# Kernel optimization log

Measured on AMD Instinct MI355X. Metric: run time of the kernel, lower is better.

Reference implementation:

```python
import jax, jax.numpy as jnp
import numpy as np

B, S, D, H = 4, 2048, 1024, 16
HD = D // H
THETA = 10000.0


def rope(x, pos, theta=THETA):
    # x: [..., seq, d], pos: broadcastable to [..., seq]
    d = x.shape[-1]
    half = d // 2
    inv_freq = 1.0 / (theta ** (jnp.arange(half, dtype=jnp.float32) * 2.0 / d))  # [half]
    ang = pos[..., None].astype(jnp.float32) * inv_freq  # [..., seq, half]
    cos, sin = jnp.cos(ang), jnp.sin(ang)
    x1, x2 = x[..., 0::2], x[..., 1::2]
    r1 = x1 * cos - x2 * sin
    r2 = x1 * sin + x2 * cos
    return jnp.stack([r1, r2], axis=-1).reshape(x.shape).astype(x.dtype)


def setup_inputs() -> dict:
    key = jax.random.key(0)
    ks = jax.random.split(key, 5)
    x = jax.random.normal(ks[0], (B, S, D), dtype=jnp.float32)
    token_positions = jnp.tile(jnp.arange(S, dtype=jnp.int64 if jax.config.jax_enable_x64 else jnp.int32), (B, 1))
    scale = 0.02
    Wq = jax.random.normal(ks[1], (D, D), dtype=jnp.float32) * scale
    Wk = jax.random.normal(ks[2], (D, D), dtype=jnp.float32) * scale
    Wv = jax.random.normal(ks[3], (D, D), dtype=jnp.float32) * scale
    Wo = jax.random.normal(ks[4], (D, D), dtype=jnp.float32) * scale
    return {"x": x, "token_positions": token_positions, "Wq": Wq, "Wk": Wk, "Wv": Wv, "Wo": Wo}


def reference(x, token_positions, Wq, Wk, Wv, Wo):
    b, s, d = x.shape
    # QKV projections (torch Linear: x @ W.T), split heads -> [b, h, s, hd]
    def proj(W):
        y = jnp.einsum('bsd,ed->bse', x, W)
        return y.reshape(b, s, H, HD).transpose(0, 2, 1, 3)
    Q, K, V = proj(Wq), proj(Wk), proj(Wv)
    # token_positions [..., seq] -> [..., 1, seq] to broadcast over heads
    pos = token_positions[:, None, :]  # [b, 1, s]
    Q = rope(Q, pos)
    K = rope(K, pos)
    # causal mask and scaled dot-product attention
    idx = jnp.arange(s)
    causal = idx[:, None] >= idx[None, :]  # [s, s], query >= key
    scores = jnp.einsum('bhqd,bhkd->bhqk', Q, K) / jnp.sqrt(jnp.float32(HD))
    scores = jnp.where(causal, scores, -jnp.inf)
    weights = jax.nn.softmax(scores, axis=-1)
    o = jnp.einsum('bhqk,bhkd->bhqd', weights, V)
    o = o.transpose(0, 2, 1, 3).reshape(b, s, d)  # merge heads
    return jnp.einsum('bsd,ed->bse', o, Wo)
```

## Files before the change

kernel.cpp:

```cpp
#include <hip/hip_runtime.h>

#define S_LEN 2048
#define NH 16
#define HDIM 64
#define DMODEL 1024

typedef __attribute__((ext_vector_type(8))) short bf16x8;
typedef __attribute__((ext_vector_type(4))) float f32x4;

__device__ __forceinline__ short f2bf(float f) {
    union { float f; unsigned u; } x; x.f = f;
    unsigned r = x.u + 0x7fffu + ((x.u >> 16) & 1u);
    return (short)(r >> 16);
}

#define GLDS(g, l) __builtin_amdgcn_global_load_lds( \
    (__attribute__((address_space(1))) void*)(g),    \
    (__attribute__((address_space(3))) void*)(l), 16, 0, 0)

#define QSCALE 0.18033688011112042f
#define FREQ_L 0.41524101186109327f

__global__ __launch_bounds__(256) void prep(const float* __restrict__ x,
                                            const float* __restrict__ wq,
                                            const float* __restrict__ wk,
                                            const float* __restrict__ wv,
                                            const float* __restrict__ wo,
                                            const int* __restrict__ tp,
                                            short* __restrict__ xb,
                                            short* __restrict__ wqb,
                                            short* __restrict__ wkb,
                                            short* __restrict__ wvb,
                                            short* __restrict__ wob,
                                            float2* __restrict__ tab) {
    int bid = blockIdx.x;
    if (bid < 8192) {
        int i = bid * 256 + threadIdx.x;
        float4 v = ((const float4*)x)[i];
        short4 o;
        o.x = f2bf(v.x); o.y = f2bf(v.y); o.z = f2bf(v.z); o.w = f2bf(v.w);
        ((short4*)xb)[i] = o;
    } else if (bid < 12288) {
        int sel = (bid - 8192) >> 10;
        const float* in = sel == 0 ? wq : sel == 1 ? wk : sel == 2 ? wv : wo;
        short* out = sel == 0 ? wqb : sel == 1 ? wkb : sel == 2 ? wvb : wob;
        int i = ((bid - 8192) & 1023) * 256 + threadIdx.x;
        float4 v = ((const float4*)in)[i];
        short4 o;
        o.x = f2bf(v.x); o.y = f2bf(v.y); o.z = f2bf(v.z); o.w = f2bf(v.w);
        ((short4*)out)[i] = o;
    } else {
        int idx = (bid - 12288) * 256 + threadIdx.x;
        int b = idx >> 16, s = (idx >> 5) & 2047, i = idx & 31;
        float p = (float)tp[(b << 11) + s];
        float freq = exp2f(-(float)i * FREQ_L);
        float sn, cs;
        sincosf(p * freq, &sn, &cs);
        tab[idx] = make_float2(cs, sn);
    }
}

__global__ __launch_bounds__(512) void gemm_qkv(const short* __restrict__ A,
                                                const short* __restrict__ Bq,
                                                const short* __restrict__ Bk,
                                                const short* __restrict__ Bv,
                                                const float2* __restrict__ tab,
                                                short* __restrict__ Qo,
                                                short* __restrict__ Ko,
                                                short* __restrict__ Vo) {
    constexpr int K = 1024;
    __shared__ __align__(16) short smem[3 * 12288];

    const int bm = blockIdx.x;
    const int sel = blockIdx.y >> 3;
    const int bn = blockIdx.y & 7;
    const short* Bm = sel == 0 ? Bq : sel == 1 ? Bk : Bv;
    short* Cb = sel == 0 ? Qo : sel == 1 ? Ko : Vo;

    const int tid = threadIdx.x;
    const int lane = tid & 63;
    const int w = tid >> 6;
    const int wm = w >> 1;
    const int wn = w & 1;
    const int quad = lane >> 4, l16 = lane & 15;

    int aoff[2], boffv;
#pragma unroll
    for (int i = 0; i < 2; i++) {
        int Lc = i * 512 + tid;
        int row = Lc >> 2;
        int gc = (Lc & 3) ^ ((row >> 1) & 3);
        aoff[i] = (bm * 256 + row) * K + gc * 8;
    }
    {
        int row = tid >> 2;
        int gc = (tid & 3) ^ ((row >> 1) & 3);
        boffv = (bn * 128 + row) * K + gc * 8;
    }

    auto stage = [&](int h, int slot) {
        char* sbase = (char*)smem + slot * 24576;
        const int kh = h * 32;
#pragma unroll
        for (int i = 0; i < 2; i++)
            GLDS(A + aoff[i] + kh, sbase + i * 8192 + w * 1024);
        GLDS(Bm + boffv + kh, sbase + 16384 + w * 1024);
    };

    f32x4 acc[4][4] = {};
    const int rsw = (quad ^ ((l16 >> 1) & 3)) * 8;

    auto compute = [&](int slot) {
        const short* sA = smem + slot * 12288;
        const short* sB = sA + 8192;
        bf16x8 af[4], bfm[4];
#pragma unroll
        for (int mi = 0; mi < 4; mi++)
            af[mi] = *(const bf16x8*)&sA[(wm * 64 + mi * 16 + l16) * 32 + rsw];
#pragma unroll
        for (int ni = 0; ni < 4; ni++)
            bfm[ni] = *(const bf16x8*)&sB[(wn * 64 + ni * 16 + l16) * 32 + rsw];
        __builtin_amdgcn_s_setprio(1);
#pragma unroll
        for (int mi = 0; mi < 4; mi++)
#pragma unroll
            for (int ni = 0; ni < 4; ni++)
                acc[mi][ni] = __builtin_amdgcn_mfma_f32_16x16x32_bf16(af[mi], bfm[ni],
                                                                      acc[mi][ni], 0, 0, 0);
        __builtin_amdgcn_s_setprio(0);
    };

    stage(0, 0); stage(1, 1);

    auto step = [&](int h, int sc, int ss) {
        asm volatile("s_waitcnt vmcnt(3)" ::: "memory");
        __builtin_amdgcn_s_barrier();
        __builtin_amdgcn_sched_barrier(0);
        stage(h + 2, ss);
        compute(sc);
    };

    for (int h = 0; h < 30; h += 3) {
        step(h + 0, 0, 2);
        step(h + 1, 1, 0);
        step(h + 2, 2, 1);
    }
    asm volatile("s_waitcnt vmcnt(3)" ::: "memory");
    __builtin_amdgcn_s_barrier();
    __builtin_amdgcn_sched_barrier(0);
    compute(0);
    asm volatile("s_waitcnt vmcnt(0)" ::: "memory");
    __builtin_amdgcn_s_barrier();
    __builtin_amdgcn_sched_barrier(0);
    compute(1);

    const int gm0 = bm * 256 + wm * 64;
    const int gn0 = bn * 128 + wn * 64;

    if (sel == 2) {
        short* T = smem;
        __syncthreads();
#pragma unroll
        for (int mi = 0; mi < 4; mi++) {
            int lmb = wm * 64 + mi * 16 + quad * 4;
#pragma unroll
            for (int ni = 0; ni < 4; ni++) {
                int ln = wn * 64 + ni * 16 + l16;
                short4 pk;
                pk.x = f2bf(acc[mi][ni][0]);
                pk.y = f2bf(acc[mi][ni][1]);
                pk.z = f2bf(acc[mi][ni][2]);
                pk.w = f2bf(acc[mi][ni][3]);
                *(short4*)&T[ln * 256 + (lmb ^ ((ln & 31) << 3))] = pk;
            }
        }
        __syncthreads();
        const int row = tid >> 2, qt = tid & 3;
        const int grow = bn * 128 + row;
        const int gb = bm >> 3;
        const int gs0 = (bm & 7) * 256;
        short* dst = Cb + (((size_t)(gb * NH + (grow >> 6)) * HDIM + (grow & 63)) * S_LEN
                           + gs0 + qt * 64);
#pragma unroll
        for (int j = 0; j < 8; j++) {
            bf16x8 v = *(const bf16x8*)&T[row * 256 +
                        ((qt * 64 + j * 8) ^ ((row & 31) << 3))];
            *(bf16x8*)(dst + j * 8) = v;
        }
    } else {
        const float qs = (sel == 0) ? QSCALE : 1.0f;
#pragma unroll
        for (int mi = 0; mi < 4; mi++)
#pragma unroll
            for (int r = 0; r < 4; r++) {
                int gm = gm0 + mi * 16 + quad * 4 + r;
                const float2* trow = tab + (gm << 5);
                int b = gm >> 11, s = gm & 2047;
#pragma unroll
                for (int ni = 0; ni < 4; ni++) {
                    float2 cs = trow[ni * 8 + (l16 >> 1)];
                    float v = acc[mi][ni][r];
                    float prt = __shfl_xor(v, 1, 64);
                    float val = (l16 & 1) ? (prt * cs.y + v * cs.x)
                                          : (v * cs.x - prt * cs.y);
                    int gn = gn0 + ni * 16 + l16;
                    int h = gn >> 6, hd = gn & 63;
                    Cb[((b * NH + h) * S_LEN + s) * HDIM + hd] = f2bf(val * qs);
                }
            }
    }
}

__global__ __launch_bounds__(512) void gemm_o(const short* __restrict__ A,
                                              const short* __restrict__ Bw,
                                              float* __restrict__ Cf) {
    constexpr int K = 1024, N = 1024;
    __shared__ __align__(16) short smem[3 * 8192];

    const int bm = blockIdx.x;
    const int bn = blockIdx.y;

    const int tid = threadIdx.x;
    const int lane = tid & 63;
    const int w = tid >> 6;
    const int wm = w >> 2;
    const int wn = w & 3;
    const int quad = lane >> 4, l16 = lane & 15;

    int aoffv, boffv;
    {
        int row = tid >> 2;
        int gc = (tid & 3) ^ ((row >> 1) & 3);
        aoffv = (bm * 128 + row) * K + gc * 8;
        boffv = (bn * 128 + row) * K + gc * 8;
    }

    auto stage = [&](int h, int slot) {
        char* sbase = (char*)smem + slot * 16384;
        const int kh = h * 32;
        GLDS(A + aoffv + kh, sbase + w * 1024);
        GLDS(Bw + boffv + kh, sbase + 8192 + w * 1024);
    };

    f32x4 acc[4][2] = {};
    const int rsw = (quad ^ ((l16 >> 1) & 3)) * 8;

    auto compute = [&](int slot) {
        const short* sA = smem + slot * 8192;
        const short* sB = sA + 4096;
        bf16x8 af[4], bfm[2];
#pragma unroll
        for (int mi = 0; mi < 4; mi++)
            af[mi] = *(const bf16x8*)&sA[(wm * 64 + mi * 16 + l16) * 32 + rsw];
#pragma unroll
        for (int ni = 0; ni < 2; ni++)
            bfm[ni] = *(const bf16x8*)&sB[(wn * 32 + ni * 16 + l16) * 32 + rsw];
        __builtin_amdgcn_s_setprio(1);
#pragma unroll
        for (int mi = 0; mi < 4; mi++)
#pragma unroll
            for (int ni = 0; ni < 2; ni++)
                acc[mi][ni] = __builtin_amdgcn_mfma_f32_16x16x32_bf16(af[mi], bfm[ni],
                                                                      acc[mi][ni], 0, 0, 0);
        __builtin_amdgcn_s_setprio(0);
    };

    stage(0, 0); stage(1, 1);

    auto step = [&](int h, int sc, int ss) {
        asm volatile("s_waitcnt vmcnt(2)" ::: "memory");
        __builtin_amdgcn_s_barrier();
        __builtin_amdgcn_sched_barrier(0);
        stage(h + 2, ss);
        compute(sc);
    };

    for (int h = 0; h < 30; h += 3) {
        step(h + 0, 0, 2);
        step(h + 1, 1, 0);
        step(h + 2, 2, 1);
    }
    asm volatile("s_waitcnt vmcnt(2)" ::: "memory");
    __builtin_amdgcn_s_barrier();
    __builtin_amdgcn_sched_barrier(0);
    compute(0);
    asm volatile("s_waitcnt vmcnt(0)" ::: "memory");
    __builtin_amdgcn_s_barrier();
    __builtin_amdgcn_sched_barrier(0);
    compute(1);

    const int gm0 = bm * 128 + wm * 64;
    const int gn0 = bn * 128 + wn * 32;
#pragma unroll
    for (int mi = 0; mi < 4; mi++)
#pragma unroll
        for (int ni = 0; ni < 2; ni++)
#pragma unroll
            for (int r = 0; r < 4; r++) {
                int gm = gm0 + mi * 16 + quad * 4 + r;
                int gn = gn0 + ni * 16 + l16;
                Cf[gm * N + gn] = acc[mi][ni][r];
            }
}

__global__ __launch_bounds__(256, 2) void attn(const short* __restrict__ Q,
                                               const short* __restrict__ Km,
                                               const short* __restrict__ Vt,
                                               short* __restrict__ O) {
    __shared__ __align__(16) short kbuf[3][64 * 64];
    __shared__ __align__(16) short vbuf[3][64 * 64];
    __shared__ __align__(16) short pbuf[4][32 * 64];

    const int lane = threadIdx.x & 63;
    const int w = threadIdx.x >> 6;
    const int quad = lane >> 4, l16 = lane & 15;
    const int l7 = l16 & 7;
    const int bh = blockIdx.x;

    const short* Qg = Q  + bh * S_LEN * 64;
    const short* Kg = Km + bh * S_LEN * 64;
    const short* Vg = Vt + bh * 64 * S_LEN;
    short* myp = &pbuf[w][0];

    const int b = bh >> 4, h = bh & 15;

    bf16x8 ones;
#pragma unroll
    for (int j = 0; j < 8; j++) ones[j] = (short)0x3f80;

    auto stage = [&](int kt, int slot) {
        const short* kt_base = Kg + kt * 64 * 64;
        const short* vt_base = Vg + kt * 64;
#pragma unroll
        for (int i = 0; i < 2; ++i) {
            int ch = w * 128 + i * 64 + lane;
            int row = ch >> 3;
            int c = (ch & 7) ^ (row & 7);
            GLDS(kt_base + row * 64 + c * 8, (char*)&kbuf[slot][(w * 128 + i * 64) * 8]);
        }
#pragma unroll
        for (int i = 0; i < 2; ++i) {
            int ch = w * 128 + i * 64 + lane;
            int row = ch >> 3;
            int c = (ch & 7) ^ (row & 7);
            GLDS(vt_base + row * S_LEN + c * 8, (char*)&vbuf[slot][(w * 128 + i * 64) * 8]);
        }
    };

    const int QtA = blockIdx.y;
    const int QtB = 15 - blockIdx.y;

    bf16x8 apA[2][2], apB[2][2];
    int s0 = 0;
    stage(0, 0);

    for (int phase = 0; phase < 2; ++phase) {
        const int Qt = phase ? QtB : QtA;
        const int nkt = 2 * Qt + 2;

        bf16x8 aq[2][2];
#pragma unroll
        for (int mi = 0; mi < 2; mi++) {
            int qrow = Qt * 128 + w * 32 + mi * 16 + l16;
#pragma unroll
            for (int kc = 0; kc < 2; kc++)
                aq[mi][kc] = *(const bf16x8*)&Qg[qrow * 64 + kc * 32 + quad * 8];
        }

        f32x4 oacc[2][4] = {};
        f32x4 lacc[2] = {};

        auto iter = [&](int kt, int scur, int snext, int sprev,
                        bf16x8 (&apc)[2][2], bf16x8 (&app)[2][2], bool hasPrev) {
            __syncthreads();
            int stk = kt + 1;
            if (stk < nkt)       stage(stk, snext);
            else if (phase == 0) stage(0,   snext);
            const short* kb = &kbuf[scur][0];
            const short* vb = &vbuf[sprev][0];

            f32x4 sc[2][4] = {};
            __builtin_amdgcn_s_setprio(1);
#pragma unroll
            for (int nt = 0; nt < 4; nt++) {
                int raddr = (nt * 16 + l16) * 64;
#pragma unroll
                for (int kc = 0; kc < 2; kc++) {
                    bf16x8 kf = *(const bf16x8*)&kb[raddr + (((quad + kc * 4) ^ l7) * 8)];
                    sc[0][nt] = __builtin_amdgcn_mfma_f32_16x16x32_bf16(aq[0][kc], kf, sc[0][nt], 0, 0, 0);
                    sc[1][nt] = __builtin_amdgcn_mfma_f32_16x16x32_bf16(aq[1][kc], kf, sc[1][nt], 0, 0, 0);
                }
            }
            if (hasPrev) {
#pragma unroll
                for (int nt = 0; nt < 4; nt++) {
                    int raddr = (nt * 16 + l16) * 64;
#pragma unroll
                    for (int kc = 0; kc < 2; kc++) {
                        bf16x8 vf = *(const bf16x8*)&vb[raddr + (((quad + kc * 4) ^ l7) * 8)];
                        oacc[0][nt] = __builtin_amdgcn_mfma_f32_16x16x32_bf16(app[0][kc], vf, oacc[0][nt], 0, 0, 0);
                        oacc[1][nt] = __builtin_amdgcn_mfma_f32_16x16x32_bf16(app[1][kc], vf, oacc[1][nt], 0, 0, 0);
                    }
                }
#pragma unroll
                for (int mi = 0; mi < 2; mi++) {
                    lacc[mi] = __builtin_amdgcn_mfma_f32_16x16x32_bf16(app[mi][0], ones, lacc[mi], 0, 0, 0);
                    lacc[mi] = __builtin_amdgcn_mfma_f32_16x16x32_bf16(app[mi][1], ones, lacc[mi], 0, 0, 0);
                }
            }
            __builtin_amdgcn_s_setprio(0);

            if (kt >= nkt - 2) {
#pragma unroll
                for (int mi = 0; mi < 2; mi++)
#pragma unroll
                    for (int nt = 0; nt < 4; nt++)
#pragma unroll
                        for (int r = 0; r < 4; r++) {
                            int col = kt * 64 + nt * 16 + l16;
                            int row = Qt * 128 + w * 32 + mi * 16 + quad * 4 + r;
                            if (col > row) sc[mi][nt][r] = -__builtin_inff();
                        }
            }
#pragma unroll
            for (int mi = 0; mi < 2; mi++)
#pragma unroll
                for (int nt = 0; nt < 4; nt++)
#pragma unroll
                    for (int r = 0; r < 4; r++) {
                        float pv = __builtin_amdgcn_exp2f(sc[mi][nt][r]);
                        int q = mi * 16 + quad * 4 + r;
                        union { float f; unsigned short us[2]; } uu;
                        uu.f = pv;
                        myp[q * 64 + (((nt * 2 + (l16 >> 3)) ^ (q & 7)) * 8) + l7] =
                            (short)uu.us[1];
                    }
#pragma unroll
            for (int mi = 0; mi < 2; mi++)
#pragma unroll
                for (int kc = 0; kc < 2; kc++)
                    apc[mi][kc] = *(const bf16x8*)&myp[(mi * 16 + l16) * 64 +
                                                       (((quad + kc * 4) ^ l7) * 8)];
        };

        for (int kt = 0; kt < nkt; kt += 2) {
            int s1 = s0 + 1; if (s1 == 3) s1 = 0;
            int s2 = s1 + 1; if (s2 == 3) s2 = 0;
            iter(kt,     s0, s1, s2, apA, apB, kt > 0);
            iter(kt + 1, s1, s2, s0, apB, apA, true);
            s0 = s2;
        }
        {
            int slast = s0 - 1; if (slast < 0) slast = 2;
            const short* vb = &vbuf[slast][0];
            __builtin_amdgcn_s_setprio(1);
#pragma unroll
            for (int nt = 0; nt < 4; nt++) {
                int raddr = (nt * 16 + l16) * 64;
#pragma unroll
                for (int kc = 0; kc < 2; kc++) {
                    bf16x8 vf = *(const bf16x8*)&vb[raddr + (((quad + kc * 4) ^ l7) * 8)];
                    oacc[0][nt] = __builtin_amdgcn_mfma_f32_16x16x32_bf16(apB[0][kc], vf, oacc[0][nt], 0, 0, 0);
                    oacc[1][nt] = __builtin_amdgcn_mfma_f32_16x16x32_bf16(apB[1][kc], vf, oacc[1][nt], 0, 0, 0);
                }
            }
#pragma unroll
            for (int mi = 0; mi < 2; mi++) {
                lacc[mi] = __builtin_amdgcn_mfma_f32_16x16x32_bf16(apB[mi][0], ones, lacc[mi], 0, 0, 0);
                lacc[mi] = __builtin_amdgcn_mfma_f32_16x16x32_bf16(apB[mi][1], ones, lacc[mi], 0, 0, 0);
            }
            __builtin_amdgcn_s_setprio(0);
        }
#pragma unroll
        for (int mi = 0; mi < 2; mi++)
#pragma unroll
            for (int r = 0; r < 4; r++) {
                float inv = 1.0f / lacc[mi][r];
                int srow = Qt * 128 + w * 32 + mi * 16 + quad * 4 + r;
#pragma unroll
                for (int nt = 0; nt < 4; nt++) {
                    int hd = nt * 16 + l16;
                    O[(b * S_LEN + srow) * DMODEL + h * HDIM + hd] = f2bf(oacc[mi][nt][r] * inv);
                }
            }
    }
}

extern "C" void kernel_launch(void* const* d_in, const int* in_sizes, int n_in,
                              void* d_out, int out_size, void* d_ws, size_t ws_size,
                              hipStream_t stream) {
    const float* x  = (const float*)d_in[0];
    const int*   tp = (const int*)d_in[1];
    const float* Wq = (const float*)d_in[2];
    const float* Wk = (const float*)d_in[3];
    const float* Wv = (const float*)d_in[4];
    const float* Wo = (const float*)d_in[5];
    float* out = (float*)d_out;

    char* ws = (char*)d_ws;
    const size_t MB = 1024 * 1024;
    short* xb  = (short*)(ws);
    short* wqb = (short*)(ws + 16 * MB);
    short* wkb = (short*)(ws + 18 * MB);
    short* wvb = (short*)(ws + 20 * MB);
    short* wob = (short*)(ws + 22 * MB);
    short* Qb  = (short*)(ws + 24 * MB);
    short* Kb  = (short*)(ws + 40 * MB);
    short* Vtb = (short*)(ws + 56 * MB);
    float2* tab = (float2*)d_out;

    prep<<<13312, 256, 0, stream>>>(x, Wq, Wk, Wv, Wo, tp,
                                    xb, wqb, wkb, wvb, wob, tab);

    gemm_qkv<<<dim3(32, 24), 512, 0, stream>>>(xb, wqb, wkb, wvb, tab, Qb, Kb, Vtb);

    attn<<<dim3(64, 8), 256, 0, stream>>>(Qb, Kb, Vtb, xb);

    gemm_o<<<dim3(64, 8), 512, 0, stream>>>(xb, wob, out);
}
```

Before: 235.1 us.

## Split attention into one query tile per block with double-buffered K/V

The attention kernel previously had each block handle two paired query tiles (Qt and 15-Qt) for load balance, with a three-slot K/V ring and a software-pipelined P·V stage lagging one iteration. It now launches 16 blocks per head, one query tile each, uses two K/V buffers, and runs QK, softmax and PV in the same iteration. Launch bounds rise to 3 blocks per CU to use the freed shared memory. The goal is more occupancy and parallelism, but it gives up the paired-tile load balancing and the overlap of PV with the next QK, and puts the K/V load for the next tile directly behind the barrier.

```diff
diff --git a/kernel.cpp b/kernel.cpp
--- a/kernel.cpp
+++ b/kernel.cpp
@@ -303,12 +303,12 @@
             }
 }
 
-__global__ __launch_bounds__(256, 2) void attn(const short* __restrict__ Q,
+__global__ __launch_bounds__(256, 3) void attn(const short* __restrict__ Q,
                                                const short* __restrict__ Km,
                                                const short* __restrict__ Vt,
                                                short* __restrict__ O) {
-    __shared__ __align__(16) short kbuf[3][64 * 64];
-    __shared__ __align__(16) short vbuf[3][64 * 64];
+    __shared__ __align__(16) short kbuf[2][64 * 64];
+    __shared__ __align__(16) short vbuf[2][64 * 64];
     __shared__ __align__(16) short pbuf[4][32 * 64];
 
     const int lane = threadIdx.x & 63;
@@ -328,7 +328,7 @@
 #pragma unroll
     for (int j = 0; j < 8; j++) ones[j] = (short)0x3f80;
 
-    auto stage = [&](int kt, int slot) {
+    auto stage = [&](int kt, int par) {
         const short* kt_base = Kg + kt * 64 * 64;
         const short* vt_base = Vg + kt * 64;
 #pragma unroll
@@ -336,154 +336,115 @@
             int ch = w * 128 + i * 64 + lane;
             int row = ch >> 3;
             int c = (ch & 7) ^ (row & 7);
-            GLDS(kt_base + row * 64 + c * 8, (char*)&kbuf[slot][(w * 128 + i * 64) * 8]);
+            GLDS(kt_base + row * 64 + c * 8, (char*)&kbuf[par][(w * 128 + i * 64) * 8]);
         }
 #pragma unroll
         for (int i = 0; i < 2; ++i) {
             int ch = w * 128 + i * 64 + lane;
             int row = ch >> 3;
             int c = (ch & 7) ^ (row & 7);
-            GLDS(vt_base + row * S_LEN + c * 8, (char*)&vbuf[slot][(w * 128 + i * 64) * 8]);
-        }
-    };
-
-    const int QtA = blockIdx.y;
-    const int QtB = 15 - blockIdx.y;
-
-    bf16x8 apA[2][2], apB[2][2];
-    int s0 = 0;
+            GLDS(vt_base + row * S_LEN + c * 8, (char*)&vbuf[par][(w * 128 + i * 64) * 8]);
+        }
+    };
+
+    const int Qt = 15 - blockIdx.y;
+    const int nkt = 2 * Qt + 2;
+
     stage(0, 0);
 
-    for (int phase = 0; phase < 2; ++phase) {
-        const int Qt = phase ? QtB : QtA;
-        const int nkt = 2 * Qt + 2;
-
-        bf16x8 aq[2][2];
+    bf16x8 aq[2][2];
+#pragma unroll
+    for (int mi = 0; mi < 2; mi++) {
+        int qrow = Qt * 128 + w * 32 + mi * 16 + l16;
+#pragma unroll
+        for (int kc = 0; kc < 2; kc++)
+            aq[mi][kc] = *(const bf16x8*)&Qg[qrow * 64 + kc * 32 + quad * 8];
+    }
+
+    f32x4 oacc[2][4] = {};
+    f32x4 lacc[2] = {};
+
+    for (int kt = 0; kt < nkt; ++kt) {
+        __syncthreads();
+        if (kt + 1 < nkt) stage(kt + 1, (kt + 1) & 1);
+        const short* kb_cur = &kbuf[kt & 1][0];
+        const short* vb_cur = &vbuf[kt & 1][0];
+
+        f32x4 sc[2][4] = {};
+        __builtin_amdgcn_s_setprio(1);
+#pragma unroll
+        for (int nt = 0; nt < 4; nt++) {
+            int raddr = (nt * 16 + l16) * 64;
+#pragma unroll
+            for (int kc = 0; kc < 2; kc++) {
+                bf16x8 kf = *(const bf16x8*)&kb_cur[raddr + (((quad + kc * 4) ^ l7) * 8)];
+                sc[0][nt] = __builtin_amdgcn_mfma_f32_16x16x32_bf16(aq[0][kc], kf, sc[0][nt], 0, 0, 0);
+                sc[1][nt] = __builtin_amdgcn_mfma_f32_16x16x32_bf16(aq[1][kc], kf, sc[1][nt], 0, 0, 0);
+            }
+        }
+        __builtin_amdgcn_s_setprio(0);
+        if (kt >= nkt - 2) {
+#pragma unroll
+            for (int mi = 0; mi < 2; mi++)
+#pragma unroll
+                for (int nt = 0; nt < 4; nt++)
+#pragma unroll
+                    for (int r = 0; r < 4; r++) {
+                        int col = kt * 64 + nt * 16 + l16;
+                        int row = Qt * 128 + w * 32 + mi * 16 + quad * 4 + r;
+                        if (col > row) sc[mi][nt][r] = -__builtin_inff();
+                    }
+        }
+#pragma unroll
+        for (int mi = 0; mi < 2; mi++)
+#pragma unroll
+            for (int nt = 0; nt < 4; nt++)
+#pragma unroll
+                for (int r = 0; r < 4; r++) {
+                    float pv = __builtin_amdgcn_exp2f(sc[mi][nt][r]);
+                    int q = mi * 16 + quad * 4 + r;
+                    union { float f; unsigned short us[2]; } uu;
+                    uu.f = pv;
+                    myp[q * 64 + (((nt * 2 + (l16 >> 3)) ^ (q & 7)) * 8) + l7] =
+                        (short)uu.us[1];
+                }
+        bf16x8 ap[2][2];
+#pragma unroll
+        for (int mi = 0; mi < 2; mi++)
+#pragma unroll
+            for (int kc = 0; kc < 2; kc++)
+                ap[mi][kc] = *(const bf16x8*)&myp[(mi * 16 + l16) * 64 +
+                                                  (((quad + kc * 4) ^ l7) * 8)];
+        __builtin_amdgcn_s_setprio(1);
+#pragma unroll
+        for (int nt = 0; nt < 4; nt++) {
+            int raddr = (nt * 16 + l16) * 64;
+#pragma unroll
+            for (int kc = 0; kc < 2; kc++) {
+                bf16x8 vf = *(const bf16x8*)&vb_cur[raddr + (((quad + kc * 4) ^ l7) * 8)];
+                oacc[0][nt] = __builtin_amdgcn_mfma_f32_16x16x32_bf16(ap[0][kc], vf, oacc[0][nt], 0, 0, 0);
+                oacc[1][nt] = __builtin_amdgcn_mfma_f32_16x16x32_bf16(ap[1][kc], vf, oacc[1][nt], 0, 0, 0);
+            }
+        }
 #pragma unroll
         for (int mi = 0; mi < 2; mi++) {
-            int qrow = Qt * 128 + w * 32 + mi * 16 + l16;
-#pragma unroll
-            for (int kc = 0; kc < 2; kc++)
-                aq[mi][kc] = *(const bf16x8*)&Qg[qrow * 64 + kc * 32 + quad * 8];
-        }
-
-        f32x4 oacc[2][4] = {};
-        f32x4 lacc[2] = {};
-
-        auto iter = [&](int kt, int scur, int snext, int sprev,
-                        bf16x8 (&apc)[2][2], bf16x8 (&app)[2][2], bool hasPrev) {
-            __syncthreads();
-            int stk = kt + 1;
-            if (stk < nkt)       stage(stk, snext);
-            else if (phase == 0) stage(0,   snext);
-            const short* kb = &kbuf[scur][0];
-            const short* vb = &vbuf[sprev][0];
-
-            f32x4 sc[2][4] = {};
-            __builtin_amdgcn_s_setprio(1);
+            lacc[mi] = __builtin_amdgcn_mfma_f32_16x16x32_bf16(ap[mi][0], ones, lacc[mi], 0, 0, 0);
+            lacc[mi] = __builtin_amdgcn_mfma_f32_16x16x32_bf16(ap[mi][1], ones, lacc[mi], 0, 0, 0);
+        }
+        __builtin_amdgcn_s_setprio(0);
+    }
+#pragma unroll
+    for (int mi = 0; mi < 2; mi++)
+#pragma unroll
+        for (int r = 0; r < 4; r++) {
+            float inv = 1.0f / lacc[mi][r];
+            int srow = Qt * 128 + w * 32 + mi * 16 + quad * 4 + r;
 #pragma unroll
             for (int nt = 0; nt < 4; nt++) {
-                int raddr = (nt * 16 + l16) * 64;
-#pragma unroll
-                for (int kc = 0; kc < 2; kc++) {
-                    bf16x8 kf = *(const bf16x8*)&kb[raddr + (((quad + kc * 4) ^ l7) * 8)];
-                    sc[0][nt] = __builtin_amdgcn_mfma_f32_16x16x32_bf16(aq[0][kc], kf, sc[0][nt], 0, 0, 0);
-                    sc[1][nt] = __builtin_amdgcn_mfma_f32_16x16x32_bf16(aq[1][kc], kf, sc[1][nt], 0, 0, 0);
-                }
-            }
-            if (hasPrev) {
-#pragma unroll
-                for (int nt = 0; nt < 4; nt++) {
-                    int raddr = (nt * 16 + l16) * 64;
-#pragma unroll
-                    for (int kc = 0; kc < 2; kc++) {
-                        bf16x8 vf = *(const bf16x8*)&vb[raddr + (((quad + kc * 4) ^ l7) * 8)];
-                        oacc[0][nt] = __builtin_amdgcn_mfma_f32_16x16x32_bf16(app[0][kc], vf, oacc[0][nt], 0, 0, 0);
-                        oacc[1][nt] = __builtin_amdgcn_mfma_f32_16x16x32_bf16(app[1][kc], vf, oacc[1][nt], 0, 0, 0);
-                    }
-                }
-#pragma unroll
-                for (int mi = 0; mi < 2; mi++) {
-                    lacc[mi] = __builtin_amdgcn_mfma_f32_16x16x32_bf16(app[mi][0], ones, lacc[mi], 0, 0, 0);
-                    lacc[mi] = __builtin_amdgcn_mfma_f32_16x16x32_bf16(app[mi][1], ones, lacc[mi], 0, 0, 0);
-                }
-            }
-            __builtin_amdgcn_s_setprio(0);
-
-            if (kt >= nkt - 2) {
-#pragma unroll
-                for (int mi = 0; mi < 2; mi++)
-#pragma unroll
-                    for (int nt = 0; nt < 4; nt++)
-#pragma unroll
-                        for (int r = 0; r < 4; r++) {
-                            int col = kt * 64 + nt * 16 + l16;
-                            int row = Qt * 128 + w * 32 + mi * 16 + quad * 4 + r;
-                            if (col > row) sc[mi][nt][r] = -__builtin_inff();
-                        }
-            }
-#pragma unroll
-            for (int mi = 0; mi < 2; mi++)
-#pragma unroll
-                for (int nt = 0; nt < 4; nt++)
-#pragma unroll
-                    for (int r = 0; r < 4; r++) {
-                        float pv = __builtin_amdgcn_exp2f(sc[mi][nt][r]);
-                        int q = mi * 16 + quad * 4 + r;
-                        union { float f; unsigned short us[2]; } uu;
-                        uu.f = pv;
-                        myp[q * 64 + (((nt * 2 + (l16 >> 3)) ^ (q & 7)) * 8) + l7] =
-                            (short)uu.us[1];
-                    }
-#pragma unroll
-            for (int mi = 0; mi < 2; mi++)
-#pragma unroll
-                for (int kc = 0; kc < 2; kc++)
-                    apc[mi][kc] = *(const bf16x8*)&myp[(mi * 16 + l16) * 64 +
-                                                       (((quad + kc * 4) ^ l7) * 8)];
-        };
-
-        for (int kt = 0; kt < nkt; kt += 2) {
-            int s1 = s0 + 1; if (s1 == 3) s1 = 0;
-            int s2 = s1 + 1; if (s2 == 3) s2 = 0;
-            iter(kt,     s0, s1, s2, apA, apB, kt > 0);
-            iter(kt + 1, s1, s2, s0, apB, apA, true);
-            s0 = s2;
-        }
-        {
-            int slast = s0 - 1; if (slast < 0) slast = 2;
-            const short* vb = &vbuf[slast][0];
-            __builtin_amdgcn_s_setprio(1);
-#pragma unroll
-            for (int nt = 0; nt < 4; nt++) {
-                int raddr = (nt * 16 + l16) * 64;
-#pragma unroll
-                for (int kc = 0; kc < 2; kc++) {
-                    bf16x8 vf = *(const bf16x8*)&vb[raddr + (((quad + kc * 4) ^ l7) * 8)];
-                    oacc[0][nt] = __builtin_amdgcn_mfma_f32_16x16x32_bf16(apB[0][kc], vf, oacc[0][nt], 0, 0, 0);
-                    oacc[1][nt] = __builtin_amdgcn_mfma_f32_16x16x32_bf16(apB[1][kc], vf, oacc[1][nt], 0, 0, 0);
-                }
-            }
-#pragma unroll
-            for (int mi = 0; mi < 2; mi++) {
-                lacc[mi] = __builtin_amdgcn_mfma_f32_16x16x32_bf16(apB[mi][0], ones, lacc[mi], 0, 0, 0);
-                lacc[mi] = __builtin_amdgcn_mfma_f32_16x16x32_bf16(apB[mi][1], ones, lacc[mi], 0, 0, 0);
-            }
-            __builtin_amdgcn_s_setprio(0);
-        }
-#pragma unroll
-        for (int mi = 0; mi < 2; mi++)
-#pragma unroll
-            for (int r = 0; r < 4; r++) {
-                float inv = 1.0f / lacc[mi][r];
-                int srow = Qt * 128 + w * 32 + mi * 16 + quad * 4 + r;
-#pragma unroll
-                for (int nt = 0; nt < 4; nt++) {
-                    int hd = nt * 16 + l16;
-                    O[(b * S_LEN + srow) * DMODEL + h * HDIM + hd] = f2bf(oacc[mi][nt][r] * inv);
-                }
-            }
-    }
+                int hd = nt * 16 + l16;
+                O[(b * S_LEN + srow) * DMODEL + h * HDIM + hd] = f2bf(oacc[mi][nt][r] * inv);
+            }
+        }
 }
 
 extern "C" void kernel_launch(void* const* d_in, const int* in_sizes, int n_in,
@@ -514,7 +475,7 @@
 
     gemm_qkv<<<dim3(32, 24), 512, 0, stream>>>(xb, wqb, wkb, wvb, tab, Qb, Kb, Vtb);
 
-    attn<<<dim3(64, 8), 256, 0, stream>>>(Qb, Kb, Vtb, xb);
+    attn<<<dim3(64, 16), 256, 0, stream>>>(Qb, Kb, Vtb, xb);
 
     gemm_o<<<dim3(64, 8), 512, 0, stream>>>(xb, wob, out);
 }
```

Measured after the change: 230.3 us (median of 2 runs). 1.02x faster.
